# Kernel optimization log

Measured on AMD Instinct MI355X. Metric: run time of the kernel, lower is better.

## Reference

```python
import jax, jax.numpy as jnp
import numpy as np

NUM_USERS = 40000
NUM_BUSINESSES = 60000
N = NUM_USERS + NUM_BUSINESSES
HIDDEN = 128
HEADS = 4
E = 200000
BATCH = 4096
NEG_SLOPE = 0.2  # PyG GATConv default


def setup_inputs() -> dict:
    key = jax.random.key(0)
    ks = jax.random.split(key, 20)
    s = 0.05
    inp = {
        "user_table": jax.random.normal(ks[0], (NUM_USERS, HIDDEN), jnp.float32) * s,
        "business_table": jax.random.normal(ks[1], (NUM_BUSINESSES, HIDDEN), jnp.float32) * s,
        # gat1: in=HIDDEN, out=HIDDEN, heads=HEADS
        "W1": jax.random.normal(ks[2], (HIDDEN, HEADS * HIDDEN), jnp.float32) * s,
        "att_src1": jax.random.normal(ks[3], (HEADS, HIDDEN), jnp.float32) * s,
        "att_dst1": jax.random.normal(ks[4], (HEADS, HIDDEN), jnp.float32) * s,
        "b1": jnp.zeros((HEADS * HIDDEN,), jnp.float32),
        # gat2: in=HEADS*HIDDEN, out=HIDDEN, heads=1
        "W2": jax.random.normal(ks[5], (HEADS * HIDDEN, HIDDEN), jnp.float32) * s,
        "att_src2": jax.random.normal(ks[6], (1, HIDDEN), jnp.float32) * s,
        "att_dst2": jax.random.normal(ks[7], (1, HIDDEN), jnp.float32) * s,
        "b2": jnp.zeros((HIDDEN,), jnp.float32),
        # predictor MLP
        "Wp1": jax.random.normal(ks[8], (2 * HIDDEN, HIDDEN), jnp.float32) * s,
        "bp1": jnp.zeros((HIDDEN,), jnp.float32),
        "Wp2": jax.random.normal(ks[9], (HIDDEN, 1), jnp.float32) * s,
        "bp2": jnp.zeros((1,), jnp.float32),
        "user_idx": jax.random.randint(ks[10], (BATCH,), 0, NUM_USERS),
        "business_idx": jax.random.randint(ks[11], (BATCH,), 0, NUM_BUSINESSES) + NUM_USERS,
        "edge_index": jax.random.randint(ks[12], (2, E), 0, N),
    }
    return inp


def gat_conv(x, edge_index, W, att_src, att_dst, bias, heads, out_ch, num_nodes):
    # add self-loops (PyG default add_self_loops=True)
    loop = jnp.arange(num_nodes)
    src = jnp.concatenate([edge_index[0], loop])
    dst = jnp.concatenate([edge_index[1], loop])
    h = (x @ W).reshape(num_nodes, heads, out_ch)            # [N,H,C]
    a_src = jnp.einsum('nhc,hc->nh', h, att_src)             # [N,H]
    a_dst = jnp.einsum('nhc,hc->nh', h, att_dst)             # [N,H]
    e = jax.nn.leaky_relu(a_src[src] + a_dst[dst], NEG_SLOPE)  # [E',H]
    # segment softmax over destination nodes
    emax = jax.ops.segment_max(e, dst, num_segments=num_nodes)
    emax = jnp.where(jnp.isfinite(emax), emax, 0.0)
    ex = jnp.exp(e - emax[dst])
    denom = jax.ops.segment_sum(ex, dst, num_segments=num_nodes)
    alpha = ex / (denom[dst] + 1e-16)                        # [E',H]
    msg = h[src] * alpha[..., None]                          # [E',H,C]
    out = jax.ops.segment_sum(msg, dst, num_segments=num_nodes)  # [N,H,C]
    return out.reshape(num_nodes, heads * out_ch) + bias


def reference(user_table, business_table, W1, att_src1, att_dst1, b1,
              W2, att_src2, att_dst2, b2, Wp1, bp1, Wp2, bp2,
              user_idx, business_idx, edge_index):
    user_emb = user_table[user_idx]                          # [B,HIDDEN]
    business_emb = business_table[business_idx - NUM_USERS]  # [B,HIDDEN]
    x = jnp.zeros((N, HIDDEN), jnp.float32)
    x = x.at[user_idx].set(user_emb)
    x = x.at[business_idx].set(business_emb)
    x = jax.nn.relu(gat_conv(x, edge_index, W1, att_src1, att_dst1, b1, HEADS, HIDDEN, N))
    x = gat_conv(x, edge_index, W2, att_src2, att_dst2, b2, 1, HIDDEN, N)
    feats = jnp.concatenate([x[user_idx], x[business_idx]], axis=1)  # [B,2*HIDDEN]
    hidden = jax.nn.relu(feats @ Wp1 + bp1)
    rating = hidden @ Wp2 + bp2                              # [B,1]
    return rating.squeeze(-1)
```

## Files before the change

### kernel.cpp

```cpp
#include <hip/hip_runtime.h>
#include <cstdint>
#include <cstddef>

#define NU      40000
#define NBZ     60000
#define NN      100000
#define HID     128
#define NHEADS  4
#define NE      200000
#define NBATCH  4096
#define BE      (2 * NBATCH)
#define SMAX    10240
#define CAP     16
#define SLOPE   0.2f

typedef __attribute__((ext_vector_type(8))) short short8v;
typedef __attribute__((ext_vector_type(4))) float f32x4;

__device__ __forceinline__ float lrelu(float x) { return x > 0.f ? x : SLOPE * x; }
__device__ __forceinline__ unsigned short f2bf(float f) {
  unsigned u = __float_as_uint(f);
  u += 0x7FFFu + ((u >> 16) & 1u);
  return (unsigned short)(u >> 16);
}


__global__ void k_mark(const int* __restrict__ user_idx, const int* __restrict__ business_idx,
                       int* __restrict__ node2slotB, int* __restrict__ cnt) {
  int i = blockIdx.x * blockDim.x + threadIdx.x;
  if (i == 0) *cnt = 0;
  if (i >= BE) return;
  int node = (i < NBATCH) ? user_idx[i] : business_idx[i - NBATCH];
  node2slotB[node] = i + 1;
}

#define W1ATT_BLOCKS 64
#define WT_BLOCKS    640
__global__ __launch_bounds__(256)
void k_frontA(const float* __restrict__ W1, const float* __restrict__ W2,
              const float* __restrict__ Wp1,
              const float* __restrict__ att_src1, const float* __restrict__ att_dst1,
              float* __restrict__ wsrc, float* __restrict__ wdst,
              short* __restrict__ w1t, short* __restrict__ w2t, short* __restrict__ wp1t,
              const int* __restrict__ ei, const int* __restrict__ n2sB,
              int* __restrict__ flags) {
  int bid = blockIdx.x, tid = threadIdx.x;
  if (bid >= W1ATT_BLOCKS + WT_BLOCKS) {
    int e = (bid - W1ATT_BLOCKS - WT_BLOCKS) * 256 + tid;
    if (e < NE) {
      int s = ei[e], d = ei[NE + e];
      if (n2sB[d] > 0) atomicOr(&flags[s], 2);
      if (n2sB[s] > 0) atomicOr(&flags[d], 1);
    }
    return;
  }
  if (bid >= W1ATT_BLOCKS) {
    int t = (bid - W1ATT_BLOCKS) * 256 + tid;
    if (t < 65536) {
      int c = t >> 14, kn = t & 16383, k = kn >> 7, n = kn & 127;
      w1t[c * 16384 + n * 128 + k] = (short)f2bf(W1[(size_t)k * 512 + c * 128 + n]);
    } else if (t < 131072) {
      int t2 = t - 65536;
      int c = t2 >> 14, kn = t2 & 16383, k = kn >> 7, n = kn & 127;
      w2t[c * 16384 + n * 128 + k] = (short)f2bf(W2[(size_t)(c * 128 + k) * 128 + n]);
    } else if (t < 163840) {
      int t3 = t - 131072;
      int k = t3 >> 7, n = t3 & 127;
      wp1t[n * 256 + k] = (short)f2bf(Wp1[(size_t)k * HID + n]);
    }
    return;
  }
  __shared__ float red[2][2][8];
  int kk = tid >> 7, c = tid & 127;
  int k = bid * 2 + kk;
  float ps[4], pd[4];
#pragma unroll
  for (int h = 0; h < 4; ++h) {
    float wv = W1[(size_t)k * 512 + h * 128 + c];
    ps[h] = wv * att_src1[h * 128 + c];
    pd[h] = wv * att_dst1[h * 128 + c];
  }
#pragma unroll
  for (int off = 1; off < 64; off <<= 1) {
#pragma unroll
    for (int h = 0; h < 4; ++h) { ps[h] += __shfl_xor(ps[h], off); pd[h] += __shfl_xor(pd[h], off); }
  }
  int half = (tid >> 6) & 1;
  if ((tid & 63) == 0) {
#pragma unroll
    for (int h = 0; h < 4; ++h) { red[kk][half][h] = ps[h]; red[kk][half][h + 4] = pd[h]; }
  }
  __syncthreads();
  if ((tid & 127) == 0) {
#pragma unroll
    for (int h = 0; h < 4; ++h) {
      wsrc[k * 4 + h] = red[kk][0][h] + red[kk][1][h];
      wdst[k * 4 + h] = red[kk][0][h + 4] + red[kk][1][h + 4];
    }
  }
}

#define SCAL1_BLOCKS (BE / 4)
__global__ __launch_bounds__(256)
void k_mid(const float* __restrict__ user_table, const float* __restrict__ business_table,
           const int* __restrict__ user_idx, const int* __restrict__ business_idx,
           const float* __restrict__ wsrc, const float* __restrict__ wdst,
           float* __restrict__ a_src1c, float* __restrict__ a_dst1c,
           const int* __restrict__ n2sB, const int* __restrict__ flags,
           int* __restrict__ slotN, int* __restrict__ slot2node, int* __restrict__ cnt,
           int* __restrict__ fillc1, int* __restrict__ indegS,
           int* __restrict__ fillc2, int* __restrict__ indegB) {
  int bid = blockIdx.x, tid = threadIdx.x;
  if (bid >= SCAL1_BLOCKS) {
    int v = (bid - SCAL1_BLOCKS) * 256 + tid;
    if (v >= NN) return;
    if (v < SMAX) { fillc1[v] = 0; indegS[v] = 0; }
    if (v < BE)   { fillc2[v] = 0; indegB[v] = 0; }
    bool need = (n2sB[v] > 0) || ((flags[v] & 3) == 3);
    int s = -1;
    if (need) {
      s = atomicAdd(cnt, 1);
      if (s >= SMAX) s = -1;
      else slot2node[s] = v;
    }
    slotN[v] = s;
    return;
  }
  int w = bid * 4 + (tid >> 6);
  int lane = tid & 63;
  int node = (w < NBATCH) ? user_idx[w] : business_idx[w - NBATCH];
  const float* src = (w < NBATCH) ? (user_table + (size_t)node * HID)
                                  : (business_table + (size_t)(node - NU) * HID);
  float2 e = *(const float2*)(src + lane * 2);
  float4 w0s = *(const float4*)(wsrc + (lane * 2) * 4);
  float4 w1s = *(const float4*)(wsrc + (lane * 2 + 1) * 4);
  float4 w0d = *(const float4*)(wdst + (lane * 2) * 4);
  float4 w1d = *(const float4*)(wdst + (lane * 2 + 1) * 4);
  float ss[4] = {e.x * w0s.x + e.y * w1s.x, e.x * w0s.y + e.y * w1s.y,
                 e.x * w0s.z + e.y * w1s.z, e.x * w0s.w + e.y * w1s.w};
  float dd[4] = {e.x * w0d.x + e.y * w1d.x, e.x * w0d.y + e.y * w1d.y,
                 e.x * w0d.z + e.y * w1d.z, e.x * w0d.w + e.y * w1d.w};
#pragma unroll
  for (int off = 1; off < 64; off <<= 1) {
#pragma unroll
    for (int h = 0; h < 4; ++h) { ss[h] += __shfl_xor(ss[h], off); dd[h] += __shfl_xor(dd[h], off); }
  }
  if (lane == 0) {
    float4 o1 = {ss[0], ss[1], ss[2], ss[3]};
    float4 o2 = {dd[0], dd[1], dd[2], dd[3]};
    *(float4*)(a_src1c + w * 4) = o1;
    *(float4*)(a_dst1c + w * 4) = o2;
  }
}

__global__ void k_fillb(const int* __restrict__ ei, const int* __restrict__ n2sB,
                        const int* __restrict__ slotN,
                        int* __restrict__ fillc1, int* __restrict__ indegS, int* __restrict__ list1,
                        int* __restrict__ fillc2, int* __restrict__ indegB, int* __restrict__ list2) {
  int e = blockIdx.x * blockDim.x + threadIdx.x;
  if (e >= NE) return;
  int s = ei[e], d = ei[NE + e];
  int snd = slotN[d];
  if (snd >= 0) {
    atomicAdd(&indegS[snd], 1);
    int sBr = n2sB[s];
    if (sBr > 0) { int p = atomicAdd(&fillc1[snd], 1); if (p < CAP) list1[snd * CAP + p] = sBr - 1; }
  }
  int dBr = n2sB[d];
  if (dBr > 0) {
    int dB = dBr - 1;
    atomicAdd(&indegB[dB], 1);
    int sns = slotN[s];
    if (sns >= 0) { int p = atomicAdd(&fillc2[dB], 1); if (p < CAP) list2[dB * CAP + p] = sns; }
  }
}

__global__ __launch_bounds__(256)
void k_agg1emb(const int* __restrict__ slot2node, const int* __restrict__ n2sB,
               const int* __restrict__ indegS, const int* __restrict__ fillc1,
               const int* __restrict__ list1,
               const float* __restrict__ a_src1c, const float* __restrict__ a_dst1c,
               const float* __restrict__ user_table, const float* __restrict__ business_table,
               const int* __restrict__ user_idx, const int* __restrict__ business_idx,
               const int* __restrict__ cntp, short* __restrict__ eaggb) {
  int w = (blockIdx.x * blockDim.x + threadIdx.x) >> 6;
  int lane = threadIdx.x & 63;
  int M = *cntp; if (M > SMAX) M = SMAX;
  if (w >= M) return;
  int v = slot2node[w];
  int dB = n2sB[v] - 1;
  float ad[4] = {0.f, 0.f, 0.f, 0.f};
  if (dB >= 0) {
    float4 a = *(const float4*)(a_dst1c + dB * 4);
    ad[0] = a.x; ad[1] = a.y; ad[2] = a.z; ad[3] = a.w;
  }
  int ne = fillc1[w];
  int nnb = indegS[w] + 1 - ne - (dB >= 0 ? 1 : 0);
  float m[4], sum[4], ax[4], ay[4];
#pragma unroll
  for (int h = 0; h < 4; ++h) {
    if (nnb > 0) { m[h] = lrelu(ad[h]); sum[h] = (float)nnb; }
    else { m[h] = -3.0e38f; sum[h] = 0.f; }
    ax[h] = 0.f; ay[h] = 0.f;
  }
  for (int j = (dB >= 0 ? -1 : 0); j < ne; ++j) {
    int sB = (j < 0) ? dB : list1[w * CAP + j];
    float4 as4 = *(const float4*)(a_src1c + sB * 4);
    float as[4] = {as4.x, as4.y, as4.z, as4.w};
    int node = (sB < NBATCH) ? user_idx[sB] : business_idx[sB - NBATCH];
    const float* src = (sB < NBATCH) ? (user_table + (size_t)node * HID)
                                     : (business_table + (size_t)(node - NU) * HID);
    float2 e = *(const float2*)(src + lane * 2);
#pragma unroll
    for (int h = 0; h < 4; ++h) {
      float x = lrelu(as[h] + ad[h]);
      if (x > m[h]) {
        float r = __expf(m[h] - x);
        sum[h] = sum[h] * r + 1.f;
        ax[h] = ax[h] * r + e.x;
        ay[h] = ay[h] * r + e.y;
        m[h] = x;
      } else {
        float p = __expf(x - m[h]);
        sum[h] += p;
        ax[h] += p * e.x;
        ay[h] += p * e.y;
      }
    }
  }
  unsigned short* o = (unsigned short*)eaggb + (size_t)w * 512;
#pragma unroll
  for (int h = 0; h < 4; ++h) {
    float r = 1.f / (sum[h] + 1e-16f);
    unsigned lo = f2bf(ax[h] * r), hi = f2bf(ay[h] * r);
    *(unsigned*)(o + h * 128 + lane * 2) = lo | (hi << 16);
  }
}

__global__ __launch_bounds__(256)
void k_mm0(const short* __restrict__ A, const short* __restrict__ Bt,
           const float* __restrict__ bias, const int* __restrict__ cntp,
           short* __restrict__ T) {
  int M = *cntp; if (M > SMAX) M = SMAX;
  int row0 = blockIdx.x * 64;
  if (row0 >= M) return;
  int c = blockIdx.y;
  int lane = threadIdx.x & 63;
  int wid = threadIdx.x >> 6;
  int l15 = lane & 15, g = lane >> 4;
  int kq = g * 8;
  f32x4 acc[4][2];
#pragma unroll
  for (int i = 0; i < 4; ++i)
#pragma unroll
    for (int j = 0; j < 2; ++j) acc[i][j] = (f32x4){0.f, 0.f, 0.f, 0.f};

#pragma unroll
  for (int k0 = 0; k0 < 128; k0 += 32) {
    short8v av[4], bv[2];
#pragma unroll
    for (int i = 0; i < 4; ++i) {
      int rA = row0 + i * 16 + l15; if (rA >= M) rA = M - 1;
      av[i] = *(const short8v*)(A + (size_t)rA * 512 + c * 128 + k0 + kq);
    }
#pragma unroll
    for (int j = 0; j < 2; ++j) {
      int col = wid * 32 + j * 16 + l15;
      bv[j] = *(const short8v*)(Bt + ((size_t)c * 128 + col) * 128 + k0 + kq);
    }
#pragma unroll
    for (int i = 0; i < 4; ++i)
#pragma unroll
      for (int j = 0; j < 2; ++j)
        acc[i][j] = __builtin_amdgcn_mfma_f32_16x16x32_bf16(av[i], bv[j], acc[i][j], 0, 0, 0);
  }
#pragma unroll
  for (int j = 0; j < 2; ++j) {
    int col = wid * 32 + j * 16 + l15;
    float bvv = bias[c * 128 + col];
#pragma unroll
    for (int i = 0; i < 4; ++i) {
#pragma unroll
      for (int q = 0; q < 4; ++q) {
        int r = row0 + i * 16 + g * 4 + q;
        if (r < M)
          ((unsigned short*)T)[(size_t)r * 512 + c * 128 + col] = f2bf(fmaxf(acc[i][j][q] + bvv, 0.f));
      }
    }
  }
}

__global__ __launch_bounds__(256)
void k_mm1p(const short* __restrict__ T, const short* __restrict__ Bt,
            const int* __restrict__ cntp, float* __restrict__ part) {
  int M = *cntp; if (M > SMAX) M = SMAX;
  int row0 = blockIdx.x * 64;
  if (row0 >= M) return;
  int c = blockIdx.z;
  int lane = threadIdx.x & 63;
  int wid = threadIdx.x >> 6;
  int l15 = lane & 15, g = lane >> 4;
  int kq = g * 8;
  f32x4 acc[4][2];
#pragma unroll
  for (int i = 0; i < 4; ++i)
#pragma unroll
    for (int j = 0; j < 2; ++j) acc[i][j] = (f32x4){0.f, 0.f, 0.f, 0.f};

#pragma unroll
  for (int k0 = 0; k0 < 128; k0 += 32) {
    short8v av[4], bv[2];
#pragma unroll
    for (int i = 0; i < 4; ++i) {
      int rA = row0 + i * 16 + l15; if (rA >= M) rA = M - 1;
      av[i] = *(const short8v*)(T + (size_t)rA * 512 + c * 128 + k0 + kq);
    }
#pragma unroll
    for (int j = 0; j < 2; ++j) {
      int col = wid * 32 + j * 16 + l15;
      bv[j] = *(const short8v*)(Bt + ((size_t)c * 128 + col) * 128 + k0 + kq);
    }
#pragma unroll
    for (int i = 0; i < 4; ++i)
#pragma unroll
      for (int j = 0; j < 2; ++j)
        acc[i][j] = __builtin_amdgcn_mfma_f32_16x16x32_bf16(av[i], bv[j], acc[i][j], 0, 0, 0);
  }
  float* Cp = part + (size_t)c * SMAX * HID;
#pragma unroll
  for (int j = 0; j < 2; ++j) {
    int col = wid * 32 + j * 16 + l15;
#pragma unroll
    for (int i = 0; i < 4; ++i) {
#pragma unroll
      for (int q = 0; q < 4; ++q) {
        int r = row0 + i * 16 + g * 4 + q;
        if (r < M) Cp[(size_t)r * HID + col] = acc[i][j][q];
      }
    }
  }
}

__global__ __launch_bounds__(256)
void k_agg2h(const int* __restrict__ user_idx, const int* __restrict__ business_idx,
             const int* __restrict__ n2sB, const int* __restrict__ slotN,
             const int* __restrict__ indegB, const int* __restrict__ fillc2,
             const int* __restrict__ list2, const float* __restrict__ part,
             const float* __restrict__ att_src2, const float* __restrict__ att_dst2,
             const float* __restrict__ b2, short* __restrict__ x2b) {
  int w = (blockIdx.x * blockDim.x + threadIdx.x) >> 6;
  int lane = threadIdx.x & 63;
  if (w >= BE) return;
  int node = (w < NBATCH) ? user_idx[w] : business_idx[w - NBATCH];
  if (n2sB[node] != w + 1) return;
  int snd = slotN[node];
  int c0 = lane * 2;
  float as2a = att_src2[c0], as2b = att_src2[c0 + 1];
  float ad2a = att_dst2[c0], ad2b = att_dst2[c0 + 1];
  size_t offS = (size_t)snd * HID + c0;
  float2 q0 = *(const float2*)(part + offS);
  float2 q1 = *(const float2*)(part + (size_t)SMAX * HID + offS);
  float2 q2 = *(const float2*)(part + (size_t)2 * SMAX * HID + offS);
  float2 q3 = *(const float2*)(part + (size_t)3 * SMAX * HID + offS);
  float hs0 = q0.x + q1.x + q2.x + q3.x;
  float hs1 = q0.y + q1.y + q2.y + q3.y;
  float ssS = hs0 * as2a + hs1 * as2b;
  float adS = hs0 * ad2a + hs1 * ad2b;
#pragma unroll
  for (int off = 1; off < 64; off <<= 1) { ssS += __shfl_xor(ssS, off); adS += __shfl_xor(adS, off); }
  float ad = adS;
  int ne = fillc2[w];
  int nnb = indegB[w] - ne;
  float m, sum;
  if (nnb > 0) { m = lrelu(ad); sum = (float)nnb; } else { m = -3.0e38f; sum = 0.f; }
  float a0 = 0.f, a1 = 0.f;
  {
    float x = lrelu(ssS + ad);
    if (x > m) { float r = __expf(m - x); sum = sum * r + 1.f; a0 = a0 * r + hs0; a1 = a1 * r + hs1; m = x; }
    else { float p = __expf(x - m); sum += p; a0 += p * hs0; a1 += p * hs1; }
  }
  for (int j = 0; j < ne; ++j) {
    int sn = list2[w * CAP + j];
    size_t off2 = (size_t)sn * HID + c0;
    float2 p0 = *(const float2*)(part + off2);
    float2 p1 = *(const float2*)(part + (size_t)SMAX * HID + off2);
    float2 p2 = *(const float2*)(part + (size_t)2 * SMAX * HID + off2);
    float2 p3 = *(const float2*)(part + (size_t)3 * SMAX * HID + off2);
    float r0 = p0.x + p1.x + p2.x + p3.x;
    float r1 = p0.y + p1.y + p2.y + p3.y;
    float ss = r0 * as2a + r1 * as2b;
#pragma unroll
    for (int off = 1; off < 64; off <<= 1) ss += __shfl_xor(ss, off);
    float x = lrelu(ss + ad);
    if (x > m) { float r = __expf(m - x); sum = sum * r + 1.f; a0 = a0 * r + r0; a1 = a1 * r + r1; m = x; }
    else { float p = __expf(x - m); sum += p; a0 += p * r0; a1 += p * r1; }
  }
  float r = 1.f / (sum + 1e-16f);
  unsigned lo = f2bf(a0 * r + b2[c0]);
  unsigned hi = f2bf(a1 * r + b2[c0 + 1]);
  *(unsigned*)((unsigned short*)x2b + (size_t)w * HID + c0) = lo | (hi << 16);
}

__global__ __launch_bounds__(512)
void k_mlp(const short* __restrict__ x2b, const short* __restrict__ wp1t,
           const int* __restrict__ user_idx, const int* __restrict__ business_idx,
           const int* __restrict__ n2sB,
           const float* __restrict__ bp1, const float* __restrict__ Wp2,
           const float* __restrict__ bp2, float* __restrict__ out) {
  __shared__ float pout[8][16];
  int row0 = blockIdx.x * 16;
  int lane = threadIdx.x & 63;
  int w = threadIdx.x >> 6;
  int l15 = lane & 15, g = lane >> 4;
  int kq = g * 8;
  int p = row0 + l15;
  int us = n2sB[user_idx[p]] - 1;
  int bs = n2sB[business_idx[p]] - 1;
  int nn = w * 16 + l15;
  f32x4 acc = {0.f, 0.f, 0.f, 0.f};
  const short* bpw = wp1t + (size_t)nn * 256 + kq;
#pragma unroll
  for (int k0 = 0; k0 < 256; k0 += 32) {
    int slot = (k0 < 128) ? us : bs;
    short8v a = *(const short8v*)(x2b + (size_t)slot * HID + (k0 & 127) + kq);
    short8v b = *(const short8v*)(bpw + k0);
    acc = __builtin_amdgcn_mfma_f32_16x16x32_bf16(a, b, acc, 0, 0, 0);
  }
  float bpv = bp1[nn], wpv = Wp2[nn];
#pragma unroll
  for (int j = 0; j < 4; ++j) {
    float v = fmaxf(acc[j] + bpv, 0.f) * wpv;
#pragma unroll
    for (int off = 1; off < 16; off <<= 1) v += __shfl_xor(v, off);
    if (l15 == 0) pout[w][g * 4 + j] = v;
  }
  __syncthreads();
  int tid = threadIdx.x;
  if (tid < 16) {
    float s = 0.f;
#pragma unroll
    for (int q = 0; q < 8; ++q) s += pout[q][tid];
    out[row0 + tid] = s + bp2[0];
  }
}

extern "C" void kernel_launch(void* const* d_in, const int* in_sizes, int n_in,
                              void* d_out, int out_size, void* d_ws, size_t ws_size,
                              hipStream_t stream) {
  const float* user_table     = (const float*)d_in[0];
  const float* business_table = (const float*)d_in[1];
  const float* W1       = (const float*)d_in[2];
  const float* att_src1 = (const float*)d_in[3];
  const float* att_dst1 = (const float*)d_in[4];
  const float* b1       = (const float*)d_in[5];
  const float* W2       = (const float*)d_in[6];
  const float* att_src2 = (const float*)d_in[7];
  const float* att_dst2 = (const float*)d_in[8];
  const float* b2       = (const float*)d_in[9];
  const float* Wp1      = (const float*)d_in[10];
  const float* bp1      = (const float*)d_in[11];
  const float* Wp2      = (const float*)d_in[12];
  const float* bp2      = (const float*)d_in[13];
  const int* user_idx     = (const int*)d_in[14];
  const int* business_idx = (const int*)d_in[15];
  const int* ei           = (const int*)d_in[16];
  float* out = (float*)d_out;

  char* w = (char*)d_ws;
  size_t used = 0;
  auto alloc = [&](size_t bytes) -> void* {
    void* p = w + used;
    used += (bytes + 255) & ~(size_t)255;
    return p;
  };
  int*   node2slotB = (int*)alloc((size_t)NN * 4);
  int*   flags      = (int*)alloc((size_t)NN * 4);
  int*   slotN      = (int*)alloc((size_t)NN * 4);
  int*   slot2node  = (int*)alloc((size_t)SMAX * 4);
  int*   cnt        = (int*)alloc(256);
  float* wsrc       = (float*)alloc((size_t)HID * 4 * 4);
  float* wdst       = (float*)alloc((size_t)HID * 4 * 4);
  float* a_src1c    = (float*)alloc((size_t)BE * 4 * 4);
  float* a_dst1c    = (float*)alloc((size_t)BE * 4 * 4);
  int*   fillc1     = (int*)alloc((size_t)SMAX * 4);
  int*   indegS     = (int*)alloc((size_t)SMAX * 4);
  int*   list1      = (int*)alloc((size_t)SMAX * CAP * 4);
  int*   fillc2     = (int*)alloc((size_t)BE * 4);
  int*   indegB     = (int*)alloc((size_t)BE * 4);
  int*   list2      = (int*)alloc((size_t)BE * CAP * 4);
  short* w1t        = (short*)alloc((size_t)NHEADS * HID * HID * 2);
  short* w2t        = (short*)alloc((size_t)NHEADS * HID * HID * 2);
  short* wp1t       = (short*)alloc((size_t)HID * 256 * 2);
  short* eaggb      = (short*)alloc((size_t)SMAX * 512 * 2);
  short* tbufb      = (short*)alloc((size_t)SMAX * 512 * 2);
  float* part       = (float*)alloc((size_t)4 * SMAX * HID * 4);
  short* x2b        = (short*)alloc((size_t)BE * HID * 2);
  if (used > ws_size) return;

  const int T = 256;
  auto cdiv = [](int a, int b) { return (a + b - 1) / b; };

  hipMemsetAsync(node2slotB, 0, (size_t)NN * 4, stream);
  hipMemsetAsync(flags, 0, (size_t)NN * 4, stream);

  k_mark<<<cdiv(BE, T), T, 0, stream>>>(user_idx, business_idx, node2slotB, cnt);

  k_frontA<<<W1ATT_BLOCKS + WT_BLOCKS + cdiv(NE, T), T, 0, stream>>>(
      W1, W2, Wp1, att_src1, att_dst1, wsrc, wdst, w1t, w2t, wp1t,
      ei, node2slotB, flags);

  k_mid<<<SCAL1_BLOCKS + cdiv(NN, T), T, 0, stream>>>(
      user_table, business_table, user_idx, business_idx, wsrc, wdst,
      a_src1c, a_dst1c, node2slotB, flags, slotN, slot2node, cnt,
      fillc1, indegS, fillc2, indegB);

  k_fillb<<<cdiv(NE, T), T, 0, stream>>>(ei, node2slotB, slotN,
                                         fillc1, indegS, list1, fillc2, indegB, list2);

  k_agg1emb<<<cdiv(SMAX * 64, T), T, 0, stream>>>(
      slot2node, node2slotB, indegS, fillc1, list1, a_src1c, a_dst1c,
      user_table, business_table, user_idx, business_idx, cnt, eaggb);

  k_mm0<<<dim3(SMAX / 64, NHEADS), T, 0, stream>>>(eaggb, w1t, b1, cnt, tbufb);
  k_mm1p<<<dim3(SMAX / 64, 1, NHEADS), T, 0, stream>>>(tbufb, w2t, cnt, part);

  k_agg2h<<<cdiv(BE * 64, T), T, 0, stream>>>(user_idx, business_idx, node2slotB, slotN,
                                              indegB, fillc2, list2, part,
                                              att_src2, att_dst2, b2, x2b);

  k_mlp<<<NBATCH / 16, 512, 0, stream>>>(x2b, wp1t, user_idx, business_idx, node2slotB,
                                         bp1, Wp2, bp2, out);
}
```

Before: 100.4 us.

## Fuse the two per-head GEMMs through LDS and replace memsets with an init kernel

```diff
diff --git a/kernel.cpp b/kernel.cpp
--- a/kernel.cpp
+++ b/kernel.cpp
@@ -25,10 +25,16 @@
 }
 
 
+__global__ void k_init(int* __restrict__ node2slotB, int* __restrict__ flags,
+                       int* __restrict__ cnt) {
+  int i = blockIdx.x * blockDim.x + threadIdx.x;
+  if (i < NN) { node2slotB[i] = 0; flags[i] = 0; }
+  if (i == 0) *cnt = 0;
+}
+
 __global__ void k_mark(const int* __restrict__ user_idx, const int* __restrict__ business_idx,
-                       int* __restrict__ node2slotB, int* __restrict__ cnt) {
+                       int* __restrict__ node2slotB) {
   int i = blockIdx.x * blockDim.x + threadIdx.x;
-  if (i == 0) *cnt = 0;
   if (i >= BE) return;
   int node = (i < NBATCH) ? user_idx[i] : business_idx[i - NBATCH];
   node2slotB[node] = i + 1;
@@ -238,9 +244,10 @@
 }
 
 __global__ __launch_bounds__(256)
-void k_mm0(const short* __restrict__ A, const short* __restrict__ Bt,
-           const float* __restrict__ bias, const int* __restrict__ cntp,
-           short* __restrict__ T) {
+void k_mm01(const short* __restrict__ A, const short* __restrict__ W1t,
+            const short* __restrict__ W2t, const float* __restrict__ bias,
+            const int* __restrict__ cntp, float* __restrict__ part) {
+  __shared__ unsigned short Tl[64][132];
   int M = *cntp; if (M > SMAX) M = SMAX;
   int row0 = blockIdx.x * 64;
   if (row0 >= M) return;
@@ -254,7 +261,6 @@
   for (int i = 0; i < 4; ++i)
 #pragma unroll
     for (int j = 0; j < 2; ++j) acc[i][j] = (f32x4){0.f, 0.f, 0.f, 0.f};
-
 #pragma unroll
   for (int k0 = 0; k0 < 128; k0 += 32) {
     short8v av[4], bv[2];
@@ -266,7 +272,7 @@
 #pragma unroll
     for (int j = 0; j < 2; ++j) {
       int col = wid * 32 + j * 16 + l15;
-      bv[j] = *(const short8v*)(Bt + ((size_t)c * 128 + col) * 128 + k0 + kq);
+      bv[j] = *(const short8v*)(W1t + ((size_t)c * 128 + col) * 128 + k0 + kq);
     }
 #pragma unroll
     for (int i = 0; i < 4; ++i)
@@ -282,43 +288,26 @@
     for (int i = 0; i < 4; ++i) {
 #pragma unroll
       for (int q = 0; q < 4; ++q) {
-        int r = row0 + i * 16 + g * 4 + q;
-        if (r < M)
-          ((unsigned short*)T)[(size_t)r * 512 + c * 128 + col] = f2bf(fmaxf(acc[i][j][q] + bvv, 0.f));
+        int r = i * 16 + g * 4 + q;
+        Tl[r][col] = f2bf(fmaxf(acc[i][j][q] + bvv, 0.f));
       }
     }
   }
-}
-
-__global__ __launch_bounds__(256)
-void k_mm1p(const short* __restrict__ T, const short* __restrict__ Bt,
-            const int* __restrict__ cntp, float* __restrict__ part) {
-  int M = *cntp; if (M > SMAX) M = SMAX;
-  int row0 = blockIdx.x * 64;
-  if (row0 >= M) return;
-  int c = blockIdx.z;
-  int lane = threadIdx.x & 63;
-  int wid = threadIdx.x >> 6;
-  int l15 = lane & 15, g = lane >> 4;
-  int kq = g * 8;
-  f32x4 acc[4][2];
+  __syncthreads();
 #pragma unroll
   for (int i = 0; i < 4; ++i)
 #pragma unroll
     for (int j = 0; j < 2; ++j) acc[i][j] = (f32x4){0.f, 0.f, 0.f, 0.f};
-
 #pragma unroll
   for (int k0 = 0; k0 < 128; k0 += 32) {
     short8v av[4], bv[2];
 #pragma unroll
-    for (int i = 0; i < 4; ++i) {
-      int rA = row0 + i * 16 + l15; if (rA >= M) rA = M - 1;
-      av[i] = *(const short8v*)(T + (size_t)rA * 512 + c * 128 + k0 + kq);
-    }
+    for (int i = 0; i < 4; ++i)
+      av[i] = *(const short8v*)&Tl[i * 16 + l15][k0 + kq];
 #pragma unroll
     for (int j = 0; j < 2; ++j) {
       int col = wid * 32 + j * 16 + l15;
-      bv[j] = *(const short8v*)(Bt + ((size_t)c * 128 + col) * 128 + k0 + kq);
+      bv[j] = *(const short8v*)(W2t + ((size_t)c * 128 + col) * 128 + k0 + kq);
     }
 #pragma unroll
     for (int i = 0; i < 4; ++i)
@@ -362,8 +351,8 @@
   float2 q1 = *(const float2*)(part + (size_t)SMAX * HID + offS);
   float2 q2 = *(const float2*)(part + (size_t)2 * SMAX * HID + offS);
   float2 q3 = *(const float2*)(part + (size_t)3 * SMAX * HID + offS);
-  float hs0 = q0.x + q1.x + q2.x + q3.x;
-  float hs1 = q0.y + q1.y + q2.y + q3.y;
+  float hs0 = (q0.x + q1.x) + (q2.x + q3.x);
+  float hs1 = (q0.y + q1.y) + (q2.y + q3.y);
   float ssS = hs0 * as2a + hs1 * as2b;
   float adS = hs0 * ad2a + hs1 * ad2b;
 #pragma unroll
@@ -386,8 +375,8 @@
     float2 p1 = *(const float2*)(part + (size_t)SMAX * HID + off2);
     float2 p2 = *(const float2*)(part + (size_t)2 * SMAX * HID + off2);
     float2 p3 = *(const float2*)(part + (size_t)3 * SMAX * HID + off2);
-    float r0 = p0.x + p1.x + p2.x + p3.x;
-    float r1 = p0.y + p1.y + p2.y + p3.y;
+    float r0 = (p0.x + p1.x) + (p2.x + p3.x);
+    float r1 = (p0.y + p1.y) + (p2.y + p3.y);
     float ss = r0 * as2a + r1 * as2b;
 #pragma unroll
     for (int off = 1; off < 64; off <<= 1) ss += __shfl_xor(ss, off);
@@ -492,18 +481,15 @@
   short* w2t        = (short*)alloc((size_t)NHEADS * HID * HID * 2);
   short* wp1t       = (short*)alloc((size_t)HID * 256 * 2);
   short* eaggb      = (short*)alloc((size_t)SMAX * 512 * 2);
-  short* tbufb      = (short*)alloc((size_t)SMAX * 512 * 2);
-  float* part       = (float*)alloc((size_t)4 * SMAX * HID * 4);
+  float* part       = (float*)alloc((size_t)NHEADS * SMAX * HID * 4);
   short* x2b        = (short*)alloc((size_t)BE * HID * 2);
   if (used > ws_size) return;
 
   const int T = 256;
   auto cdiv = [](int a, int b) { return (a + b - 1) / b; };
 
-  hipMemsetAsync(node2slotB, 0, (size_t)NN * 4, stream);
-  hipMemsetAsync(flags, 0, (size_t)NN * 4, stream);
-
-  k_mark<<<cdiv(BE, T), T, 0, stream>>>(user_idx, business_idx, node2slotB, cnt);
+  k_init<<<cdiv(NN, T), T, 0, stream>>>(node2slotB, flags, cnt);
+  k_mark<<<cdiv(BE, T), T, 0, stream>>>(user_idx, business_idx, node2slotB);
 
   k_frontA<<<W1ATT_BLOCKS + WT_BLOCKS + cdiv(NE, T), T, 0, stream>>>(
       W1, W2, Wp1, att_src1, att_dst1, wsrc, wdst, w1t, w2t, wp1t,
@@ -521,8 +507,7 @@
       slot2node, node2slotB, indegS, fillc1, list1, a_src1c, a_dst1c,
       user_table, business_table, user_idx, business_idx, cnt, eaggb);
 
-  k_mm0<<<dim3(SMAX / 64, NHEADS), T, 0, stream>>>(eaggb, w1t, b1, cnt, tbufb);
-  k_mm1p<<<dim3(SMAX / 64, 1, NHEADS), T, 0, stream>>>(tbufb, w2t, cnt, part);
+  k_mm01<<<dim3(SMAX / 64, NHEADS), T, 0, stream>>>(eaggb, w1t, w2t, b1, cnt, part);
 
   k_agg2h<<<cdiv(BE * 64, T), T, 0, stream>>>(user_idx, business_idx, node2slotB, slotN,
                                               indegB, fillc2, list2, part,
```

Measured after the change: 85.73 us (median of 2 runs). -14.6%, faster.
